# Performance work log

Hardware: AMD Instinct MI355X
Metric: run time of the kernel (lower is better)

## Reference

```python
import jax, jax.numpy as jnp
import numpy as np

HEADS = 4
KS = 7          # neighborhood kernel size
EPS = 1e-5
C = 64
N, H, W = 8, 64, 64


def _gather_idx(L, k):
    # NATTEN-style neighborhood: window centered at pixel, shifted to stay in bounds.
    start = jnp.clip(jnp.arange(L) - k // 2, 0, L - k)            # [L]
    idx = start[:, None] + jnp.arange(k)                           # [L, k] absolute neighbor idx
    # relative-position-bias index: (query - neighbor) + (k-1) in [0, 2k-2]
    rel = (jnp.arange(L) - start)[:, None] + (k - 1) - jnp.arange(k)[None, :]  # [L, k]
    return idx, rel


def na2d(x, qkv_w, qkv_b, rpb, proj_w, proj_b):
    # x: [N, H, W, C] -> neighborhood attention with rel-pos bias
    n, h, w, c = x.shape
    hd = c // HEADS
    scale = hd ** -0.5
    qkv = (x @ qkv_w.T + qkv_b).reshape(n, h, w, 3, HEADS, hd)
    q = qkv[..., 0, :, :] * scale                                  # [n,h,w,heads,hd]
    k = qkv[..., 1, :, :]
    v = qkv[..., 2, :, :]
    idx_h, rel_h = _gather_idx(h, KS)
    idx_w, rel_w = _gather_idx(w, KS)
    # gather neighborhoods: [n, h, k, w, k, heads, hd]
    kg = k[:, idx_h][:, :, :, idx_w]
    vg = v[:, idx_h][:, :, :, idx_w]
    attn = jnp.einsum('nijhd,niajbhd->nijhab', q, kg)              # [n,h,w,heads,k,k]
    bias = rpb[:, rel_h, :]                                        # [heads, h, k, 2k-1]
    bias = jnp.take(bias, rel_w, axis=-1)                          # [heads, h, k, w, k]
    bias = jnp.transpose(bias, (1, 3, 0, 2, 4))                    # [h, w, heads, k, k]
    attn = attn + bias
    a = jax.nn.softmax(attn.reshape(n, h, w, HEADS, KS * KS), axis=-1).reshape(attn.shape)
    out = jnp.einsum('nijhab,niajbhd->nijhd', a, vg).reshape(n, h, w, c)
    return out @ proj_w.T + proj_b


def setup_inputs() -> dict:
    key = jax.random.key(0)
    ks = jax.random.split(key, 12)
    s = 0.02
    return {
        'x': jax.random.normal(ks[0], (N, C, H, W), jnp.float32),
        'gn_w': jnp.ones((C,), jnp.float32),
        'gn_b': jnp.zeros((C,), jnp.float32),
        'qkv_w': jax.random.normal(ks[1], (3 * C, C), jnp.float32) * s,
        'qkv_b': jnp.zeros((3 * C,), jnp.float32),
        'rpb': jax.random.normal(ks[2], (HEADS, 2 * KS - 1, 2 * KS - 1), jnp.float32) * s,
        'proj_w': jax.random.normal(ks[3], (C, C), jnp.float32) * s,
        'proj_b': jnp.zeros((C,), jnp.float32),
        'ln_w': jnp.ones((C,), jnp.float32),
        'ln_b': jnp.zeros((C,), jnp.float32),
        'fc1_w': jax.random.normal(ks[4], (4 * C, C), jnp.float32) * s,
        'fc1_b': jnp.zeros((4 * C,), jnp.float32),
        'fc2_w': jax.random.normal(ks[5], (C, 4 * C), jnp.float32) * s,
        'fc2_b': jnp.zeros((C,), jnp.float32),
    }


def reference(x, gn_w, gn_b, qkv_w, qkv_b, rpb, proj_w, proj_b,
              ln_w, ln_b, fc1_w, fc1_b, fc2_w, fc2_b):
    n, c, h, w = x.shape
    x1 = jnp.transpose(x, (0, 2, 3, 1))                            # residual, NHWC
    # GroupNorm(1, C): normalize over (C,H,W) per sample, per-channel affine
    mu = jnp.mean(x, axis=(1, 2, 3), keepdims=True)
    var = jnp.var(x, axis=(1, 2, 3), keepdims=True)
    xg = (x - mu) * jax.lax.rsqrt(var + EPS)
    xg = xg * gn_w[None, :, None, None] + gn_b[None, :, None, None]
    xg = jnp.transpose(xg, (0, 2, 3, 1))                           # NHWC
    y = na2d(xg, qkv_w, qkv_b, rpb, proj_w, proj_b) + x1           # [n,h,w,c]
    y = y.reshape(n, h * w, c)
    # LayerNorm over channels + MLP (GELU), residual
    mu2 = jnp.mean(y, axis=-1, keepdims=True)
    var2 = jnp.var(y, axis=-1, keepdims=True)
    yn = (y - mu2) * jax.lax.rsqrt(var2 + EPS) * ln_w + ln_b
    hdn = jax.nn.gelu(yn @ fc1_w.T + fc1_b, approximate=False)
    y = y + (hdn @ fc2_w.T + fc2_b)
    return jnp.transpose(y.reshape(n, h, w, c), (0, 3, 1, 2))      # back to NCHW
```

## Files before the change

kernel.cpp:

```cpp
#include <hip/hip_runtime.h>
#include <math.h>

#define NSAMP 8
#define CH 64
#define HH 64
#define WW 64
#define SPATIAL 4096
#define PER_SAMPLE 262144
#define NTOK 32768
#define NHEADS 4
#define HD 16
#define KS 7
#define EPS 1e-5f
#define QSCALE 0.25f

typedef __attribute__((ext_vector_type(8))) short short8;
typedef __attribute__((ext_vector_type(4))) float f32x4;

__device__ __forceinline__ unsigned short f2bf(float f) {
    unsigned u = __float_as_uint(f);
    u = u + 0x7fffu + ((u >> 16) & 1u);
    return (unsigned short)(u >> 16);
}
__device__ __forceinline__ unsigned pack2(float a, float b) {
    return (unsigned)f2bf(a) | ((unsigned)f2bf(b) << 16);
}
__device__ __forceinline__ float dot8_bf(uint4 u, const float* qv) {
    float s;
    s = __uint_as_float(u.x << 16) * qv[0];
    s = fmaf(__uint_as_float(u.x & 0xffff0000u), qv[1], s);
    s = fmaf(__uint_as_float(u.y << 16),         qv[2], s);
    s = fmaf(__uint_as_float(u.y & 0xffff0000u), qv[3], s);
    s = fmaf(__uint_as_float(u.z << 16),         qv[4], s);
    s = fmaf(__uint_as_float(u.z & 0xffff0000u), qv[5], s);
    s = fmaf(__uint_as_float(u.w << 16),         qv[6], s);
    s = fmaf(__uint_as_float(u.w & 0xffff0000u), qv[7], s);
    return s;
}
__device__ __forceinline__ void pv8_bf(uint4 u, float p, float* acc) {
    acc[0] = fmaf(p, __uint_as_float(u.x << 16),         acc[0]);
    acc[1] = fmaf(p, __uint_as_float(u.x & 0xffff0000u), acc[1]);
    acc[2] = fmaf(p, __uint_as_float(u.y << 16),         acc[2]);
    acc[3] = fmaf(p, __uint_as_float(u.y & 0xffff0000u), acc[3]);
    acc[4] = fmaf(p, __uint_as_float(u.z << 16),         acc[4]);
    acc[5] = fmaf(p, __uint_as_float(u.z & 0xffff0000u), acc[5]);
    acc[6] = fmaf(p, __uint_as_float(u.w << 16),         acc[6]);
    acc[7] = fmaf(p, __uint_as_float(u.w & 0xffff0000u), acc[7]);
}

__global__ __launch_bounds__(256) void k_statsprep(const float* __restrict__ x,
                                                   float* __restrict__ stats,
                                                   const float* __restrict__ qkv_w,
                                                   const float* __restrict__ fc1_w,
                                                   const float* __restrict__ fc2_w,
                                                   const float* __restrict__ proj_w,
                                                   unsigned short* __restrict__ wb) {
    int blk = blockIdx.x;
    if (blk >= 256) {
        int i = (blk - 256) * 256 + threadIdx.x;
        if (i < 12288)      wb[i] = f2bf(qkv_w[i]);
        else if (i < 28672) wb[i] = f2bf(fc1_w[i - 12288]);
        else if (i < 45056) wb[i] = f2bf(fc2_w[i - 28672]);
        else                wb[i] = f2bf(proj_w[i - 45056]);
        return;
    }
    int n = blk >> 5, chunk = blk & 31;
    const float4* p4 = (const float4*)(x + n * PER_SAMPLE + chunk * 8192);
    int t = threadIdx.x;
    float s1 = 0.f, s2 = 0.f;
#pragma unroll
    for (int i = 0; i < 8; i++) {
        float4 v = p4[t + i * 256];
        s1 += v.x + v.y + v.z + v.w;
        s2 += v.x * v.x + v.y * v.y + v.z * v.z + v.w * v.w;
    }
#pragma unroll
    for (int off = 1; off < 64; off <<= 1) {
        s1 += __shfl_xor(s1, off);
        s2 += __shfl_xor(s2, off);
    }
    __shared__ float r1[4], r2[4];
    int lane = t & 63, wv = t >> 6;
    if (lane == 0) { r1[wv] = s1; r2[wv] = s2; }
    __syncthreads();
    if (t == 0) {
        atomicAdd(&stats[n * 2 + 0], r1[0] + r1[1] + r1[2] + r1[3]);
        atomicAdd(&stats[n * 2 + 1], r2[0] + r2[1] + r2[2] + r2[3]);
    }
}

__global__ __launch_bounds__(256) void k_qkv(const float* __restrict__ x,
                                             const float* __restrict__ stats,
                                             const float* __restrict__ gn_w,
                                             const float* __restrict__ gn_b,
                                             const unsigned short* __restrict__ qkv_wb,
                                             const float* __restrict__ qkv_b,
                                             uint4* __restrict__ qb8,
                                             uint4* __restrict__ kvb8) {
    __shared__ __attribute__((aligned(16))) short xA[4 * 2 * 64 * 8];
    __shared__ float obuf[4][16 * 65];
    int s0 = blockIdx.x * 64;
    int smp = s0 >> 12, sp = s0 & 4095;
    int t = threadIdx.x, tok = t & 63, g = t >> 6;

    float mu = stats[2 * smp] * (1.f / (float)PER_SAMPLE);
    float var = stats[2 * smp + 1] * (1.f / (float)PER_SAMPLE) - mu * mu;
    float rstd = rsqrtf(var + EPS);

    {
        const float* xp = x + smp * PER_SAMPLE + sp + tok;
        float v[16];
#pragma unroll
        for (int i = 0; i < 16; i++) {
            int c = g * 16 + i;
            v[i] = (xp[(size_t)c * SPATIAL] - mu) * rstd * gn_w[c] + gn_b[c];
        }
#pragma unroll
        for (int e = 0; e < 2; e++) {
            int cb = 2 * g + e;
            int kf = cb >> 2, qq = cb & 3;
            uint4 p;
            p.x = pack2(v[e * 8 + 0], v[e * 8 + 1]);
            p.y = pack2(v[e * 8 + 2], v[e * 8 + 3]);
            p.z = pack2(v[e * 8 + 4], v[e * 8 + 5]);
            p.w = pack2(v[e * 8 + 6], v[e * 8 + 7]);
            int chunk = ((tok >> 4) * 2 + kf) * 64 + (tok & 15) + (qq << 4);
            *(uint4*)&xA[chunk * 8] = p;
        }
    }
    __syncthreads();

    int w = __builtin_amdgcn_readfirstlane(g);
    int lane = t & 63, nh = lane & 15, qd = lane >> 4;

    short8 af[8];
#pragma unroll
    for (int mt = 0; mt < 4; mt++)
#pragma unroll
        for (int kf = 0; kf < 2; kf++)
            af[mt * 2 + kf] = *(const short8*)&xA[((mt * 2 + kf) * 64 + lane) * 8];

    for (int nt = 0; nt < 3; nt++) {
        int n0 = w * 48 + nt * 16;
        const unsigned short* wp = qkv_wb + (size_t)(n0 + nh) * 64 + qd * 8;
        short8 b0 = *(const short8*)(wp);
        short8 b1 = *(const short8*)(wp + 32);
        float bias = qkv_b[n0 + nh];
        bool isq = (n0 < 64);
        f32x4 acc[4];
#pragma unroll
        for (int mt = 0; mt < 4; mt++) {
            f32x4 d = {0.f, 0.f, 0.f, 0.f};
            d = __builtin_amdgcn_mfma_f32_16x16x32_bf16(af[mt * 2 + 0], b0, d, 0, 0, 0);
            d = __builtin_amdgcn_mfma_f32_16x16x32_bf16(af[mt * 2 + 1], b1, d, 0, 0, 0);
            acc[mt] = d;
        }
#pragma unroll
        for (int mt = 0; mt < 4; mt++)
#pragma unroll
            for (int r = 0; r < 4; r++) {
                float vv = acc[mt][r] + bias;
                if (isq) vv *= QSCALE;
                obuf[w][nh * 65 + mt * 16 + qd * 4 + r] = vv;
            }
        __builtin_amdgcn_wave_barrier();
#pragma unroll
        for (int u = 0; u < 2; u++) {
            uint4 p;
            p.x = pack2(obuf[w][(u * 8 + 0) * 65 + lane], obuf[w][(u * 8 + 1) * 65 + lane]);
            p.y = pack2(obuf[w][(u * 8 + 2) * 65 + lane], obuf[w][(u * 8 + 3) * 65 + lane]);
            p.z = pack2(obuf[w][(u * 8 + 4) * 65 + lane], obuf[w][(u * 8 + 5) * 65 + lane]);
            p.w = pack2(obuf[w][(u * 8 + 6) * 65 + lane], obuf[w][(u * 8 + 7) * 65 + lane]);
            if (n0 < 64)
                qb8[(size_t)((n0 >> 3) + u) * NTOK + s0 + lane] = p;
            else if (n0 < 128)
                kvb8[(size_t)(((n0 - 64) >> 3) + u) * NTOK + s0 + lane] = p;
            else
                kvb8[(size_t)(8 + ((n0 - 128) >> 3) + u) * NTOK + s0 + lane] = p;
        }
        __builtin_amdgcn_wave_barrier();
    }
}

__global__ __launch_bounds__(256, 4) void k_fused(const uint4* __restrict__ qb8,
                                               const uint4* __restrict__ kvb8,
                                               const float* __restrict__ rpb,
                                               const unsigned short* __restrict__ proj_wb,
                                               const float* __restrict__ proj_b,
                                               const float* __restrict__ x,
                                               const float* __restrict__ ln_w,
                                               const float* __restrict__ ln_b,
                                               const unsigned short* __restrict__ fc1_wb,
                                               const float* __restrict__ fc1_b,
                                               const unsigned short* __restrict__ fc2_wb,
                                               const float* __restrict__ fc2_b,
                                               float* __restrict__ out) {
    __shared__ __attribute__((aligned(16))) short fragA[2 * 2 * 64 * 8];
    __shared__ __attribute__((aligned(16))) short lhA[2 * 8 * 64 * 8];
    __shared__ float obuf[4][16 * 33];
    __shared__ float red1[256], red2[256];
    int xcd = blockIdx.x & 7, idx = blockIdx.x >> 3;
    int half = idx & 1;
    int h = xcd * 8 + ((idx >> 1) & 7);
    int n = idx >> 4;
    int t = threadIdx.x, lane = t & 63;
    int g = __builtin_amdgcn_readfirstlane(t >> 6);
    int w2 = lane & 31;
    int dh = lane >> 5;
    int w = half * 32 + w2;
    int rowbase = n * 4096 + h * 64;
    int cb = 2 * g + dh;

    const float* xr = x + n * PER_SAMPLE + h * 64 + w;
    float xres[8];
#pragma unroll
    for (int i = 0; i < 8; i++)
        xres[i] = xr[(size_t)(cb * 8 + i) * SPATIAL];

    float q[8];
    {
        uint4 qa = qb8[(size_t)cb * NTOK + rowbase + w];
        q[0] = __uint_as_float(qa.x << 16); q[1] = __uint_as_float(qa.x & 0xffff0000u);
        q[2] = __uint_as_float(qa.y << 16); q[3] = __uint_as_float(qa.y & 0xffff0000u);
        q[4] = __uint_as_float(qa.z << 16); q[5] = __uint_as_float(qa.z & 0xffff0000u);
        q[6] = __uint_as_float(qa.w << 16); q[7] = __uint_as_float(qa.w & 0xffff0000u);
    }
    int sh = min(max(h - 3, 0), HH - KS);
    int sw = min(max(w - 3, 0), WW - KS);

    float sum = 0.f;
    float acc[8];
#pragma unroll
    for (int i = 0; i < 8; i++) acc[i] = 0.f;

#pragma unroll
    for (int a = 0; a < 7; a++) {
        int nb = n * 4096 + (sh + a) * 64 + sw;
        const float* rp = rpb + (g * 13 + (h - sh + 6 - a)) * 13 + (w - sw + 6);
        const uint4* kp = kvb8 + (size_t)cb * NTOK + nb;
        const uint4* vp = kvb8 + (size_t)(8 + cb) * NTOK + nb;
#pragma unroll
        for (int bb = 0; bb < 7; bb++) {
            uint4 kv = kp[bb];
            uint4 vv = vp[bb];
            float dhalf = dot8_bf(kv, q);
            float d = dhalf + __shfl_xor(dhalf, 32);
            d += rp[-bb];
            float e = __expf(d);
            sum += e;
            pv8_bf(vv, e, acc);
        }
    }
    float rs = 1.f / sum;

    {
        int kf = cb >> 2, qsel = cb & 3;
        uint4 p;
        p.x = pack2(acc[0] * rs, acc[1] * rs);
        p.y = pack2(acc[2] * rs, acc[3] * rs);
        p.z = pack2(acc[4] * rs, acc[5] * rs);
        p.w = pack2(acc[6] * rs, acc[7] * rs);
        *(uint4*)&fragA[(((w2 >> 4) * 2 + kf) * 64 + (w2 & 15) + (qsel << 4)) * 8] = p;
    }
    __syncthreads();

    int nh = lane & 15, qd = lane >> 4;
    float yreg[8];
    {
        short8 af[4];
#pragma unroll
        for (int mt = 0; mt < 2; mt++)
#pragma unroll
            for (int kf = 0; kf < 2; kf++)
                af[mt * 2 + kf] = *(const short8*)&fragA[((mt * 2 + kf) * 64 + lane) * 8];

        int n0 = g * 16;
        const unsigned short* wp = proj_wb + (size_t)(n0 + nh) * 64 + qd * 8;
        short8 b0 = *(const short8*)(wp);
        short8 b1 = *(const short8*)(wp + 32);
        float bias = proj_b[n0 + nh];
#pragma unroll
        for (int mt = 0; mt < 2; mt++) {
            f32x4 d = {0.f, 0.f, 0.f, 0.f};
            d = __builtin_amdgcn_mfma_f32_16x16x32_bf16(af[mt * 2 + 0], b0, d, 0, 0, 0);
            d = __builtin_amdgcn_mfma_f32_16x16x32_bf16(af[mt * 2 + 1], b1, d, 0, 0, 0);
#pragma unroll
            for (int r = 0; r < 4; r++)
                obuf[g][nh * 33 + mt * 16 + qd * 4 + r] = d[r] + bias;
        }
        __builtin_amdgcn_wave_barrier();
#pragma unroll
        for (int i = 0; i < 8; i++)
            yreg[i] = obuf[g][(dh * 8 + i) * 33 + w2] + xres[i];
    }

    {
        float s1 = 0.f, s2 = 0.f;
#pragma unroll
        for (int i = 0; i < 8; i++) { s1 += yreg[i]; s2 += yreg[i] * yreg[i]; }
        red1[t] = s1;
        red2[t] = s2;
        __syncthreads();
        float m1 = 0.f, m2 = 0.f;
#pragma unroll
        for (int u = 0; u < 8; u++) { m1 += red1[u * 32 + w2]; m2 += red2[u * 32 + w2]; }
        float mu = m1 * (1.f / 64.f);
        float rstd = rsqrtf(m2 * (1.f / 64.f) - mu * mu + EPS);
        float v[8];
#pragma unroll
        for (int i = 0; i < 8; i++) {
            int c = cb * 8 + i;
            v[i] = (yreg[i] - mu) * rstd * ln_w[c] + ln_b[c];
        }
        int kf = cb >> 2, qsel = cb & 3;
        uint4 p;
        p.x = pack2(v[0], v[1]);
        p.y = pack2(v[2], v[3]);
        p.z = pack2(v[4], v[5]);
        p.w = pack2(v[6], v[7]);
        *(uint4*)&fragA[(((w2 >> 4) * 2 + kf) * 64 + (w2 & 15) + (qsel << 4)) * 8] = p;
    }
    __syncthreads();

    {
        short8 yf[4];
#pragma unroll
        for (int mt = 0; mt < 2; mt++)
#pragma unroll
            for (int kf = 0; kf < 2; kf++)
                yf[mt * 2 + kf] = *(const short8*)&fragA[((mt * 2 + kf) * 64 + lane) * 8];

#pragma unroll
        for (int nt = 0; nt < 4; nt++) {
            int n0f = g * 64 + nt * 16;
            const unsigned short* wp = fc1_wb + (size_t)(n0f + nh) * 64 + qd * 8;
            short8 b0 = *(const short8*)(wp);
            short8 b1 = *(const short8*)(wp + 32);
            float bias = fc1_b[n0f + nh];
            int j = n0f + nh;
            int kfA = j >> 5, q2 = (j >> 3) & 3, jb = j & 7;
#pragma unroll
            for (int mt = 0; mt < 2; mt++) {
                f32x4 d = {0.f, 0.f, 0.f, 0.f};
                d = __builtin_amdgcn_mfma_f32_16x16x32_bf16(yf[mt * 2 + 0], b0, d, 0, 0, 0);
                d = __builtin_amdgcn_mfma_f32_16x16x32_bf16(yf[mt * 2 + 1], b1, d, 0, 0, 0);
#pragma unroll
                for (int r = 0; r < 4; r++) {
                    float hv = d[r] + bias;
                    hv = 0.5f * hv * (1.f + erff(hv * 0.70710678118654752f));
                    lhA[((mt * 8 + kfA) * 64 + (qd * 4 + r) + (q2 << 4)) * 8 + jb] = (short)f2bf(hv);
                }
            }
        }
    }
    __syncthreads();

    f32x4 acc2[2];
    acc2[0] = (f32x4){0.f, 0.f, 0.f, 0.f};
    acc2[1] = (f32x4){0.f, 0.f, 0.f, 0.f};
#pragma unroll
    for (int kfA = 0; kfA < 8; kfA++) {
        const unsigned short* wp = fc2_wb + (size_t)(g * 16 + nh) * 256 + kfA * 32 + qd * 8;
        short8 bb = *(const short8*)(wp);
#pragma unroll
        for (int mt = 0; mt < 2; mt++) {
            short8 a = *(const short8*)&lhA[((mt * 8 + kfA) * 64 + lane) * 8];
            acc2[mt] = __builtin_amdgcn_mfma_f32_16x16x32_bf16(a, bb, acc2[mt], 0, 0, 0);
        }
    }
#pragma unroll
    for (int mt = 0; mt < 2; mt++)
#pragma unroll
        for (int r = 0; r < 4; r++)
            obuf[g][nh * 33 + mt * 16 + qd * 4 + r] = acc2[mt][r];
    __builtin_amdgcn_wave_barrier();
    float* op = out + (size_t)n * PER_SAMPLE + h * 64 + w;
#pragma unroll
    for (int i = 0; i < 8; i++) {
        int c = cb * 8 + i;
        op[(size_t)c * SPATIAL] = obuf[g][(dh * 8 + i) * 33 + w2] + fc2_b[c] + yreg[i];
    }
}

extern "C" void kernel_launch(void* const* d_in, const int* in_sizes, int n_in,
                              void* d_out, int out_size, void* d_ws, size_t ws_size,
                              hipStream_t stream) {
    const float* x      = (const float*)d_in[0];
    const float* gn_w   = (const float*)d_in[1];
    const float* gn_b   = (const float*)d_in[2];
    const float* qkv_w  = (const float*)d_in[3];
    const float* qkv_b  = (const float*)d_in[4];
    const float* rpb    = (const float*)d_in[5];
    const float* proj_w = (const float*)d_in[6];
    const float* proj_b = (const float*)d_in[7];
    const float* ln_w   = (const float*)d_in[8];
    const float* ln_b   = (const float*)d_in[9];
    const float* fc1_w  = (const float*)d_in[10];
    const float* fc1_b  = (const float*)d_in[11];
    const float* fc2_w  = (const float*)d_in[12];
    const float* fc2_b  = (const float*)d_in[13];
    float* out = (float*)d_out;

    float* ws    = (float*)d_ws;
    float* stats = ws;
    uint4* qb8   = (uint4*)(ws + 64);
    uint4* kvb8  = qb8 + (size_t)8 * NTOK;
    unsigned short* wb = (unsigned short*)(kvb8 + (size_t)16 * NTOK);
    unsigned short* qkv_wb  = wb;
    unsigned short* fc1_wb  = wb + 12288;
    unsigned short* fc2_wb  = wb + 28672;
    unsigned short* proj_wb = wb + 45056;

    hipMemsetAsync(stats, 0, 64, stream);
    k_statsprep<<<448, 256, 0, stream>>>(x, stats, qkv_w, fc1_w, fc2_w, proj_w, wb);
    k_qkv      <<<512, 256, 0, stream>>>(x, stats, gn_w, gn_b, qkv_wb, qkv_b, qb8, kvb8);
    k_fused    <<<1024, 256, 0, stream>>>(qb8, kvb8, rpb, proj_wb, proj_b, x,
                                          ln_w, ln_b, fc1_wb, fc1_b, fc2_wb, fc2_b, out);
}
```

Baseline: 129.9 us.

## Halve QKV tile to 32 tokens and remap blocks to XCDs by image row

The QKV projection kernel now processes 32 tokens per block instead of 64, doubling the grid to 1024 blocks for more parallelism. The block index is decoded so that each XCD handles a contiguous band of image rows, which is meant to improve L2 locality for the later neighborhood-attention reads. The change adds per-block overhead such as weight loads and barriers over half as much work, and the smaller obuf shrinks shared memory.

Measured after the change: 132.9 us. +2.3%, slower.

```diff
diff --git a/kernel.cpp b/kernel.cpp
--- a/kernel.cpp
+++ b/kernel.cpp
@@ -97,86 +97,77 @@
                                              const float* __restrict__ qkv_b,
                                              uint4* __restrict__ qb8,
                                              uint4* __restrict__ kvb8) {
-    __shared__ __attribute__((aligned(16))) short xA[4 * 2 * 64 * 8];
-    __shared__ float obuf[4][16 * 65];
-    int s0 = blockIdx.x * 64;
-    int smp = s0 >> 12, sp = s0 & 4095;
-    int t = threadIdx.x, tok = t & 63, g = t >> 6;
-
-    float mu = stats[2 * smp] * (1.f / (float)PER_SAMPLE);
-    float var = stats[2 * smp + 1] * (1.f / (float)PER_SAMPLE) - mu * mu;
+    __shared__ __attribute__((aligned(16))) short fragA[2 * 2 * 64 * 8];
+    __shared__ float obuf[4][16 * 33];
+    int xcd = blockIdx.x & 7, idx = blockIdx.x >> 3;
+    int half = idx & 1;
+    int h = xcd * 8 + ((idx >> 1) & 7);
+    int n = idx >> 4;
+    int t = threadIdx.x, lane = t & 63;
+    int g = __builtin_amdgcn_readfirstlane(t >> 6);
+    int s0 = n * 4096 + h * 64 + half * 32;
+    int nh = lane & 15, qd = lane >> 4;
+
+    float mu = stats[2 * n] * (1.f / (float)PER_SAMPLE);
+    float var = stats[2 * n + 1] * (1.f / (float)PER_SAMPLE) - mu * mu;
     float rstd = rsqrtf(var + EPS);
 
     {
-        const float* xp = x + smp * PER_SAMPLE + sp + tok;
-        float v[16];
-#pragma unroll
-        for (int i = 0; i < 16; i++) {
-            int c = g * 16 + i;
+        int tok32 = t & 31, cbq = t >> 5;
+        const float* xp = x + n * PER_SAMPLE + h * 64 + half * 32 + tok32;
+        float v[8];
+#pragma unroll
+        for (int i = 0; i < 8; i++) {
+            int c = cbq * 8 + i;
             v[i] = (xp[(size_t)c * SPATIAL] - mu) * rstd * gn_w[c] + gn_b[c];
         }
-#pragma unroll
-        for (int e = 0; e < 2; e++) {
-            int cb = 2 * g + e;
-            int kf = cb >> 2, qq = cb & 3;
-            uint4 p;
-            p.x = pack2(v[e * 8 + 0], v[e * 8 + 1]);
-            p.y = pack2(v[e * 8 + 2], v[e * 8 + 3]);
-            p.z = pack2(v[e * 8 + 4], v[e * 8 + 5]);
-            p.w = pack2(v[e * 8 + 6], v[e * 8 + 7]);
-            int chunk = ((tok >> 4) * 2 + kf) * 64 + (tok & 15) + (qq << 4);
-            *(uint4*)&xA[chunk * 8] = p;
-        }
+        int kf = cbq >> 2, qsel = cbq & 3;
+        uint4 p;
+        p.x = pack2(v[0], v[1]);
+        p.y = pack2(v[2], v[3]);
+        p.z = pack2(v[4], v[5]);
+        p.w = pack2(v[6], v[7]);
+        *(uint4*)&fragA[(((tok32 >> 4) * 2 + kf) * 64 + (tok32 & 15) + (qsel << 4)) * 8] = p;
     }
     __syncthreads();
 
-    int w = __builtin_amdgcn_readfirstlane(g);
-    int lane = t & 63, nh = lane & 15, qd = lane >> 4;
-
-    short8 af[8];
-#pragma unroll
-    for (int mt = 0; mt < 4; mt++)
+    short8 af[4];
+#pragma unroll
+    for (int mt = 0; mt < 2; mt++)
 #pragma unroll
         for (int kf = 0; kf < 2; kf++)
-            af[mt * 2 + kf] = *(const short8*)&xA[((mt * 2 + kf) * 64 + lane) * 8];
+            af[mt * 2 + kf] = *(const short8*)&fragA[((mt * 2 + kf) * 64 + lane) * 8];
 
     for (int nt = 0; nt < 3; nt++) {
-        int n0 = w * 48 + nt * 16;
+        int n0 = g * 48 + nt * 16;
         const unsigned short* wp = qkv_wb + (size_t)(n0 + nh) * 64 + qd * 8;
         short8 b0 = *(const short8*)(wp);
         short8 b1 = *(const short8*)(wp + 32);
         float bias = qkv_b[n0 + nh];
         bool isq = (n0 < 64);
-        f32x4 acc[4];
-#pragma unroll
-        for (int mt = 0; mt < 4; mt++) {
+#pragma unroll
+        for (int mt = 0; mt < 2; mt++) {
             f32x4 d = {0.f, 0.f, 0.f, 0.f};
             d = __builtin_amdgcn_mfma_f32_16x16x32_bf16(af[mt * 2 + 0], b0, d, 0, 0, 0);
             d = __builtin_amdgcn_mfma_f32_16x16x32_bf16(af[mt * 2 + 1], b1, d, 0, 0, 0);
-            acc[mt] = d;
-        }
-#pragma unroll
-        for (int mt = 0; mt < 4; mt++)
 #pragma unroll
             for (int r = 0; r < 4; r++) {
-                float vv = acc[mt][r] + bias;
+                float vv = d[r] + bias;
                 if (isq) vv *= QSCALE;
-                obuf[w][nh * 65 + mt * 16 + qd * 4 + r] = vv;
+                obuf[g][nh * 33 + mt * 16 + qd * 4 + r] = vv;
             }
+        }
         __builtin_amdgcn_wave_barrier();
-#pragma unroll
-        for (int u = 0; u < 2; u++) {
+        {
+            int tok = lane & 31, u = lane >> 5;
             uint4 p;
-            p.x = pack2(obuf[w][(u * 8 + 0) * 65 + lane], obuf[w][(u * 8 + 1) * 65 + lane]);
-            p.y = pack2(obuf[w][(u * 8 + 2) * 65 + lane], obuf[w][(u * 8 + 3) * 65 + lane]);
-            p.z = pack2(obuf[w][(u * 8 + 4) * 65 + lane], obuf[w][(u * 8 + 5) * 65 + lane]);
-            p.w = pack2(obuf[w][(u * 8 + 6) * 65 + lane], obuf[w][(u * 8 + 7) * 65 + lane]);
-            if (n0 < 64)
-                qb8[(size_t)((n0 >> 3) + u) * NTOK + s0 + lane] = p;
-            else if (n0 < 128)
-                kvb8[(size_t)(((n0 - 64) >> 3) + u) * NTOK + s0 + lane] = p;
-            else
-                kvb8[(size_t)(8 + ((n0 - 128) >> 3) + u) * NTOK + s0 + lane] = p;
+            p.x = pack2(obuf[g][(u * 8 + 0) * 33 + tok], obuf[g][(u * 8 + 1) * 33 + tok]);
+            p.y = pack2(obuf[g][(u * 8 + 2) * 33 + tok], obuf[g][(u * 8 + 3) * 33 + tok]);
+            p.z = pack2(obuf[g][(u * 8 + 4) * 33 + tok], obuf[g][(u * 8 + 5) * 33 + tok]);
+            p.w = pack2(obuf[g][(u * 8 + 6) * 33 + tok], obuf[g][(u * 8 + 7) * 33 + tok]);
+            int row = (n0 >> 3) + u;
+            if (n0 < 64) qb8[(size_t)row * NTOK + s0 + tok] = p;
+            else         kvb8[(size_t)(row - 8) * NTOK + s0 + tok] = p;
         }
         __builtin_amdgcn_wave_barrier();
     }
@@ -413,7 +404,7 @@
 
     hipMemsetAsync(stats, 0, 64, stream);
     k_statsprep<<<448, 256, 0, stream>>>(x, stats, qkv_w, fc1_w, fc2_w, proj_w, wb);
-    k_qkv      <<<512, 256, 0, stream>>>(x, stats, gn_w, gn_b, qkv_wb, qkv_b, qb8, kvb8);
+    k_qkv      <<<1024, 256, 0, stream>>>(x, stats, gn_w, gn_b, qkv_wb, qkv_b, qb8, kvb8);
     k_fused    <<<1024, 256, 0, stream>>>(qb8, kvb8, rpb, proj_wb, proj_b, x,
                                           ln_w, ln_b, fc1_wb, fc1_b, fc2_wb, fc2_b, out);
 }
```
